# Optimization experiments

Measured on AMD Instinct MI355X. Metric: run time of the kernel, lower is better.

The kernel has to match this reference:

```python
import jax, jax.numpy as jnp
import numpy as np


def setup_inputs() -> dict:
    key = jax.random.key(0)
    k1, k2 = jax.random.split(key)
    completed = jax.random.normal(k1, (8, 8192, 3), dtype=jnp.float32)
    partial = jax.random.normal(k2, (8, 4096, 3), dtype=jnp.float32)
    return {"completed": completed, "partial": partial}


def reference(completed, partial) -> jnp.ndarray:
    # torch.cdist(partial, completed): (B, M, N) pairwise Euclidean distances
    # d^2 = ||p||^2 + ||c||^2 - 2 p.c  (computed via GEMM, matching cdist math)
    p_sq = jnp.sum(partial * partial, axis=-1, keepdims=True)          # (B, M, 1)
    c_sq = jnp.sum(completed * completed, axis=-1, keepdims=True)       # (B, N, 1)
    cross = jnp.einsum("bmd,bnd->bmn", partial, completed)             # (B, M, N)
    d2 = p_sq + jnp.swapaxes(c_sq, 1, 2) - 2.0 * cross                  # (B, M, N)
    dist = jnp.sqrt(jnp.maximum(d2, 0.0))
    min_dist = jnp.min(dist, axis=2)                                    # (B, M)
    return jnp.mean(min_dist)
```

## Files before the change

### kernel.cpp

```cpp
#include <hip/hip_runtime.h>


constexpr int B  = 8;
constexpr int N  = 8192;
constexpr int M  = 4096;
constexpr int NT = 256;
constexpr int TP = 8;
constexpr int MBLK = NT * TP;
constexpr int MC   = M / MBLK;
constexpr int NBLK = 128;
constexpr int NC   = N / NBLK;
constexpr int ROWS = B * M;
constexpr float FMAX = 3.402823466e38f;

__global__ __launch_bounds__(NT, 4) void pml_main(const float* __restrict__ completed,
                                                  const float* __restrict__ partial,
                                                  float* __restrict__ ws,
                                                  float* __restrict__ out) {
    __shared__ float4 cs[NBLK];
    const int t     = threadIdx.x;
    const int b     = blockIdx.z;
    const int mBase = blockIdx.y * MBLK;
    const int nBase = blockIdx.x * NBLK;

    if (blockIdx.x == 0 && blockIdx.y == 0 && b == 0 && t == 0)
        out[0] = 0.0f;

    if (t < NBLK) {
        const float* cp = completed + (size_t)(b * N + nBase + t) * 3;
        float x = cp[0], y = cp[1], z = cp[2];
        cs[t] = make_float4(x, y, z, 0.5f * (x * x + y * y + z * z));
    }
    __syncthreads();

    const int m0 = mBase + t * TP;
    const float4* pv = (const float4*)(partial + (size_t)(b * M + m0) * 3);
    float4 v0 = pv[0], v1 = pv[1], v2 = pv[2], v3 = pv[3], v4 = pv[4], v5 = pv[5];

    float nx[TP], ny[TP], nz[TP], fm[TP];
    nx[0] = -v0.x; ny[0] = -v0.y; nz[0] = -v0.z;
    nx[1] = -v0.w; ny[1] = -v1.x; nz[1] = -v1.y;
    nx[2] = -v1.z; ny[2] = -v1.w; nz[2] = -v2.x;
    nx[3] = -v2.y; ny[3] = -v2.z; nz[3] = -v2.w;
    nx[4] = -v3.x; ny[4] = -v3.y; nz[4] = -v3.z;
    nx[5] = -v3.w; ny[5] = -v4.x; nz[5] = -v4.y;
    nx[6] = -v4.z; ny[6] = -v4.w; nz[6] = -v5.x;
    nx[7] = -v5.y; ny[7] = -v5.z; nz[7] = -v5.w;
#pragma unroll
    for (int p = 0; p < TP; ++p) fm[p] = FMAX;

#pragma unroll 4
    for (int j = 0; j < NBLK; j += 2) {
        float4 c0 = cs[j];
        float4 c1 = cs[j + 1];
#pragma unroll
        for (int p = 0; p < TP; ++p) {
            float f0 = fmaf(nx[p], c0.x, fmaf(ny[p], c0.y, fmaf(nz[p], c0.z, c0.w)));
            float f1 = fmaf(nx[p], c1.x, fmaf(ny[p], c1.y, fmaf(nz[p], c1.z, c1.w)));
            fm[p] = fminf(fm[p], fminf(f0, f1));
        }
    }

    float4* wsv = (float4*)(ws + (size_t)blockIdx.x * ROWS + b * M + m0);
    wsv[0] = make_float4(fm[0], fm[1], fm[2], fm[3]);
    wsv[1] = make_float4(fm[4], fm[5], fm[6], fm[7]);
}

constexpr int RT      = 64;
constexpr int RQUADS  = ROWS / 4;
constexpr int RBLOCKS = RQUADS / RT;

__global__ __launch_bounds__(RT) void pml_reduce(const float* __restrict__ ws,
                                                 const float* __restrict__ partial,
                                                 float* __restrict__ out) {
    const int q = blockIdx.x * RT + threadIdx.x;
    const float4* wsv = (const float4*)ws;

    float4 m = make_float4(FMAX, FMAX, FMAX, FMAX);
#pragma unroll 16
    for (int c = 0; c < NC; ++c) {
        float4 v = wsv[(size_t)c * RQUADS + q];
        m.x = fminf(m.x, v.x);
        m.y = fminf(m.y, v.y);
        m.z = fminf(m.z, v.z);
        m.w = fminf(m.w, v.w);
    }

    const float4* pp = (const float4*)partial + (size_t)q * 3;
    float4 a = pp[0], bb = pp[1], cc = pp[2];

    float psq0 = a.x * a.x + a.y * a.y + a.z * a.z;
    float psq1 = a.w * a.w + bb.x * bb.x + bb.y * bb.y;
    float psq2 = bb.z * bb.z + bb.w * bb.w + cc.x * cc.x;
    float psq3 = cc.y * cc.y + cc.z * cc.z + cc.w * cc.w;

    float s = sqrtf(fmaxf(fmaf(2.0f, m.x, psq0), 0.0f))
            + sqrtf(fmaxf(fmaf(2.0f, m.y, psq1), 0.0f))
            + sqrtf(fmaxf(fmaf(2.0f, m.z, psq2), 0.0f))
            + sqrtf(fmaxf(fmaf(2.0f, m.w, psq3), 0.0f));

#pragma unroll
    for (int off = 32; off > 0; off >>= 1) s += __shfl_down(s, off);

    if (threadIdx.x == 0)
        atomicAdd(out, s * (1.0f / (float)ROWS));
}

extern "C" void kernel_launch(void* const* d_in, const int* in_sizes, int n_in,
                              void* d_out, int out_size, void* d_ws, size_t ws_size,
                              hipStream_t stream) {
    const float* completed = (const float*)d_in[0];
    const float* partial   = (const float*)d_in[1];
    float* out = (float*)d_out;
    float* ws  = (float*)d_ws;

    dim3 grid(NC, MC, B);
    pml_main<<<grid, NT, 0, stream>>>(completed, partial, ws, out);
    pml_reduce<<<RBLOCKS, RT, 0, stream>>>(ws, partial, out);
}
```

Before: 82.71 us.

## Precompute packed completed points and read them directly instead of via LDS

Adds a prep kernel that packs each completed point into a float4 holding x, y, z and half its squared norm. The main kernel then drops its shared-memory staging and barrier and loads eight packed points per iteration straight from global memory. All lanes read the same addresses, so these become broadcast loads served by cache. This removes the per-block LDS fill and sync, but adds a kernel launch plus workspace traffic and relies on cached global loads being as cheap as LDS reads.

```diff
diff --git a/kernel.cpp b/kernel.cpp
--- a/kernel.cpp
+++ b/kernel.cpp
@@ -11,13 +11,25 @@
 constexpr int NBLK = 128;
 constexpr int NC   = N / NBLK;
 constexpr int ROWS = B * M;
+constexpr int PKQ  = B * N;
 constexpr float FMAX = 3.402823466e38f;
 
-__global__ __launch_bounds__(NT, 4) void pml_main(const float* __restrict__ completed,
+__global__ __launch_bounds__(256) void pml_prep(const float* __restrict__ completed,
+                                                float4* __restrict__ pk) {
+    const int i = blockIdx.x * 256 + threadIdx.x;
+    const float4* src = (const float4*)completed + (size_t)i * 3;
+    float4 a = src[0], b4 = src[1], c4 = src[2];
+    float4* dst = pk + (size_t)i * 4;
+    dst[0] = make_float4(a.x,  a.y,  a.z,  0.5f * (a.x*a.x  + a.y*a.y  + a.z*a.z));
+    dst[1] = make_float4(a.w,  b4.x, b4.y, 0.5f * (a.w*a.w  + b4.x*b4.x + b4.y*b4.y));
+    dst[2] = make_float4(b4.z, b4.w, c4.x, 0.5f * (b4.z*b4.z + b4.w*b4.w + c4.x*c4.x));
+    dst[3] = make_float4(c4.y, c4.z, c4.w, 0.5f * (c4.y*c4.y + c4.z*c4.z + c4.w*c4.w));
+}
+
+__global__ __launch_bounds__(NT, 4) void pml_main(const float4* __restrict__ pk,
                                                   const float* __restrict__ partial,
-                                                  float* __restrict__ ws,
+                                                  float* __restrict__ fminw,
                                                   float* __restrict__ out) {
-    __shared__ float4 cs[NBLK];
     const int t     = threadIdx.x;
     const int b     = blockIdx.z;
     const int mBase = blockIdx.y * MBLK;
@@ -25,13 +37,6 @@
 
     if (blockIdx.x == 0 && blockIdx.y == 0 && b == 0 && t == 0)
         out[0] = 0.0f;
-
-    if (t < NBLK) {
-        const float* cp = completed + (size_t)(b * N + nBase + t) * 3;
-        float x = cp[0], y = cp[1], z = cp[2];
-        cs[t] = make_float4(x, y, z, 0.5f * (x * x + y * y + z * z));
-    }
-    __syncthreads();
 
     const int m0 = mBase + t * TP;
     const float4* pv = (const float4*)(partial + (size_t)(b * M + m0) * 3);
@@ -49,19 +54,26 @@
 #pragma unroll
     for (int p = 0; p < TP; ++p) fm[p] = FMAX;
 
-#pragma unroll 4
-    for (int j = 0; j < NBLK; j += 2) {
-        float4 c0 = cs[j];
-        float4 c1 = cs[j + 1];
+    const float4* cp = pk + (size_t)b * N + nBase;
+
+#pragma unroll 2
+    for (int j = 0; j < NBLK; j += 8) {
+        float4 cc[8];
 #pragma unroll
-        for (int p = 0; p < TP; ++p) {
-            float f0 = fmaf(nx[p], c0.x, fmaf(ny[p], c0.y, fmaf(nz[p], c0.z, c0.w)));
-            float f1 = fmaf(nx[p], c1.x, fmaf(ny[p], c1.y, fmaf(nz[p], c1.z, c1.w)));
-            fm[p] = fminf(fm[p], fminf(f0, f1));
+        for (int k = 0; k < 8; ++k) cc[k] = cp[j + k];
+#pragma unroll
+        for (int q = 0; q < 4; ++q) {
+            const float4 c0 = cc[2 * q], c1 = cc[2 * q + 1];
+#pragma unroll
+            for (int p = 0; p < TP; ++p) {
+                float f0 = fmaf(nx[p], c0.x, fmaf(ny[p], c0.y, fmaf(nz[p], c0.z, c0.w)));
+                float f1 = fmaf(nx[p], c1.x, fmaf(ny[p], c1.y, fmaf(nz[p], c1.z, c1.w)));
+                fm[p] = fminf(fm[p], fminf(f0, f1));
+            }
         }
     }
 
-    float4* wsv = (float4*)(ws + (size_t)blockIdx.x * ROWS + b * M + m0);
+    float4* wsv = (float4*)(fminw + (size_t)blockIdx.x * ROWS + b * M + m0);
     wsv[0] = make_float4(fm[0], fm[1], fm[2], fm[3]);
     wsv[1] = make_float4(fm[4], fm[5], fm[6], fm[7]);
 }
@@ -70,14 +82,14 @@
 constexpr int RQUADS  = ROWS / 4;
 constexpr int RBLOCKS = RQUADS / RT;
 
-__global__ __launch_bounds__(RT) void pml_reduce(const float* __restrict__ ws,
+__global__ __launch_bounds__(RT) void pml_reduce(const float* __restrict__ fminw,
                                                  const float* __restrict__ partial,
                                                  float* __restrict__ out) {
     const int q = blockIdx.x * RT + threadIdx.x;
-    const float4* wsv = (const float4*)ws;
+    const float4* wsv = (const float4*)fminw;
 
     float4 m = make_float4(FMAX, FMAX, FMAX, FMAX);
-#pragma unroll 16
+#pragma unroll 8
     for (int c = 0; c < NC; ++c) {
         float4 v = wsv[(size_t)c * RQUADS + q];
         m.x = fminf(m.x, v.x);
@@ -114,7 +126,11 @@
     float* out = (float*)d_out;
     float* ws  = (float*)d_ws;
 
+    float4* pk    = (float4*)ws;
+    float*  fminw = ws + (size_t)PKQ * 4;
+
+    pml_prep<<<PKQ / 4 / 256, 256, 0, stream>>>(completed, pk);
     dim3 grid(NC, MC, B);
-    pml_main<<<grid, NT, 0, stream>>>(completed, partial, ws, out);
-    pml_reduce<<<RBLOCKS, RT, 0, stream>>>(ws, partial, out);
+    pml_main<<<grid, NT, 0, stream>>>(pk, partial, fminw, out);
+    pml_reduce<<<RBLOCKS, RT, 0, stream>>>(fminw, partial, out);
 }
```

Result: slower. 93.59 us (+13.2%).
